# Optimization experiments

Hardware: AMD Instinct MI355X
Metric: run time of the kernel (lower is better)

## Reference

```python
import jax, jax.numpy as jnp
import numpy as np

B, S, H, NH, FF = 16, 1024, 768, 12, 3072
D = H // NH  # 64
EPS = 1e-12


def layer_norm(x, g, b):
    mu = jnp.mean(x, axis=-1, keepdims=True)
    var = jnp.mean(jnp.square(x - mu), axis=-1, keepdims=True)
    return (x - mu) * jax.lax.rsqrt(var + EPS) * g + b


def setup_inputs() -> dict:
    key = jax.random.key(0)
    ks = jax.random.split(key, 16)
    w = lambda k, shape: (jax.random.normal(k, shape, jnp.float32) * 0.02)
    return {
        "features": jax.random.normal(ks[0], (B, S, H), jnp.float32),
        "attention_mask": jnp.zeros((B, S), jnp.float32),  # additive mask
        "wq": w(ks[1], (H, H)), "bq": jnp.zeros((H,), jnp.float32),
        "wk": w(ks[2], (H, H)), "bk": jnp.zeros((H,), jnp.float32),
        "wv": w(ks[3], (H, H)), "bv": jnp.zeros((H,), jnp.float32),
        "wo": w(ks[4], (H, H)), "bo": jnp.zeros((H,), jnp.float32),
        "ln1_g": jnp.ones((H,), jnp.float32), "ln1_b": jnp.zeros((H,), jnp.float32),
        "w1": w(ks[5], (H, FF)), "b1": jnp.zeros((FF,), jnp.float32),
        "w2": w(ks[6], (FF, H)), "b2": jnp.zeros((H,), jnp.float32),
        "ln2_g": jnp.ones((H,), jnp.float32), "ln2_b": jnp.zeros((H,), jnp.float32),
        "wp": w(ks[7], (H, H)), "bp": jnp.zeros((H,), jnp.float32),
        "wm": w(ks[8], (H, 1)), "bm": jnp.zeros((1,), jnp.float32),
    }


def reference(features, attention_mask, wq, bq, wk, bk, wv, bv, wo, bo,
              ln1_g, ln1_b, w1, b1, w2, b2, ln2_g, ln2_b, wp, bp, wm, bm):
    mask = attention_mask[:, None, None, :]  # [B,1,1,S]

    def split_heads(x):  # [B,S,H] -> [B,NH,S,D]
        return x.reshape(B, S, NH, D).transpose(0, 2, 1, 3)

    q = split_heads(features @ wq + bq)
    k = split_heads(features @ wk + bk)
    v = split_heads(features @ wv + bv)

    scores = jnp.einsum("bhqd,bhkd->bhqk", q, k) / np.sqrt(D).astype(np.float32)
    probs = jax.nn.softmax(scores + mask, axis=-1)  # dropout is identity (eval)
    ctx = jnp.einsum("bhqk,bhkd->bhqd", probs, v)
    ctx = ctx.transpose(0, 2, 1, 3).reshape(B, S, H)

    attn_out = layer_norm(ctx @ wo + bo + features, ln1_g, ln1_b)
    ffn = jax.nn.gelu(attn_out @ w1 + b1, approximate=False) @ w2 + b2
    hidden = layer_norm(ffn + attn_out, ln2_g, ln2_b)

    pooled = jnp.tanh(hidden[:, 0] @ wp + bp)  # BertPooler on [CLS]
    cls = (pooled @ wm + bm).squeeze()  # [B]
    return cls
```

## Files before the change

kernel.cpp:

```cpp
#include <hip/hip_runtime.h>
#include <math.h>

namespace {

constexpr int B  = 16;
constexpr int S  = 1024;
constexpr int H  = 768;
constexpr int NH = 12;
constexpr int DH = 64;
constexpr int FF = 3072;
constexpr int KSPL = 16;
constexpr float EPS = 1e-12f;

__device__ __forceinline__ float waveReduceSum(float v) {
#pragma unroll
    for (int d = 1; d < 64; d <<= 1) v += __shfl_xor(v, d);
    return v;
}

__device__ __forceinline__ float blockReduceSum768(float v, float* red) {
    const int lane = threadIdx.x & 63;
    const int wid  = threadIdx.x >> 6;
    v = waveReduceSum(v);
    __syncthreads();
    if (lane == 0) red[wid] = v;
    __syncthreads();
    float s = 0.f;
#pragma unroll
    for (int w = 0; w < 12; ++w) s += red[w];
    return s;
}

template <int K, int ISPL, int N>
__global__ __launch_bounds__(256) void gemm_partial(
        const float* __restrict__ A, int lda, int jtOfsA,
        const float* __restrict__ W, float* __restrict__ part) {
    constexpr int IR = K / ISPL;
    __shared__ float Asl[B * IR];
    const int jt  = blockIdx.x;
    const int sp  = blockIdx.y;
    const int i0  = sp * IR;
    const int tid = threadIdx.x;

    for (int e = tid; e < B * IR; e += 256) {
        const int b = e / IR, ii = e % IR;
        Asl[e] = A[(size_t)b * lda + (size_t)jt * jtOfsA + i0 + ii];
    }
    __syncthreads();

    const int jl = tid & 63;
    const int bg = tid >> 6;
    const int j  = jt * 64 + jl;
    const float* wp_ = W + (size_t)i0 * N + j;
    const float* a0 = Asl + (bg * 4 + 0) * IR;
    const float* a1 = Asl + (bg * 4 + 1) * IR;
    const float* a2 = Asl + (bg * 4 + 2) * IR;
    const float* a3 = Asl + (bg * 4 + 3) * IR;
    float acc0 = 0.f, acc1 = 0.f, acc2 = 0.f, acc3 = 0.f;
#pragma unroll
    for (int ii = 0; ii < IR; ++ii) {
        const float w = wp_[(size_t)ii * N];
        acc0 += w * a0[ii];
        acc1 += w * a1[ii];
        acc2 += w * a2[ii];
        acc3 += w * a3[ii];
    }
    float* pp = part + ((size_t)sp * B) * N + j;
    pp[(size_t)(bg * 4 + 0) * N] = acc0;
    pp[(size_t)(bg * 4 + 1) * N] = acc1;
    pp[(size_t)(bg * 4 + 2) * N] = acc2;
    pp[(size_t)(bg * 4 + 3) * N] = acc3;
}

template <int K, int ISPL, int N, int RED>
__global__ __launch_bounds__(256) void gemm_partial_red(
        const float* __restrict__ Ain, const float* __restrict__ bias,
        const float* __restrict__ W, float* __restrict__ part) {
    constexpr int IR = K / ISPL;
    __shared__ float Asl[B * IR];
    const int jt  = blockIdx.x;
    const int sp  = blockIdx.y;
    const int i0  = sp * IR;
    const int tid = threadIdx.x;

    for (int e = tid; e < B * IR; e += 256) {
        const int b = e / IR, ii = e % IR;
        float v = bias[i0 + ii];
#pragma unroll
        for (int sp2 = 0; sp2 < RED; ++sp2)
            v += Ain[((size_t)sp2 * B + b) * K + i0 + ii];
        Asl[e] = v;
    }
    __syncthreads();

    const int jl = tid & 63;
    const int bg = tid >> 6;
    const int j  = jt * 64 + jl;
    const float* wp_ = W + (size_t)i0 * N + j;
    const float* a0 = Asl + (bg * 4 + 0) * IR;
    const float* a1 = Asl + (bg * 4 + 1) * IR;
    const float* a2 = Asl + (bg * 4 + 2) * IR;
    const float* a3 = Asl + (bg * 4 + 3) * IR;
    float acc0 = 0.f, acc1 = 0.f, acc2 = 0.f, acc3 = 0.f;
#pragma unroll
    for (int ii = 0; ii < IR; ++ii) {
        const float w = wp_[(size_t)ii * N];
        acc0 += w * a0[ii];
        acc1 += w * a1[ii];
        acc2 += w * a2[ii];
        acc3 += w * a3[ii];
    }
    float* pp = part + ((size_t)sp * B) * N + j;
    pp[(size_t)(bg * 4 + 0) * N] = acc0;
    pp[(size_t)(bg * 4 + 1) * N] = acc1;
    pp[(size_t)(bg * 4 + 2) * N] = acc2;
    pp[(size_t)(bg * 4 + 3) * N] = acc3;
}

template <int K, int ISPL, int N, int RED>
__global__ __launch_bounds__(256) void gemm_partial_red_gelu(
        const float* __restrict__ Ain, const float* __restrict__ bias,
        const float* __restrict__ W, float* __restrict__ part) {
    constexpr int IR = K / ISPL;
    __shared__ float Asl[B * IR];
    const int jt  = blockIdx.x;
    const int sp  = blockIdx.y;
    const int i0  = sp * IR;
    const int tid = threadIdx.x;

    for (int e = tid; e < B * IR; e += 256) {
        const int b = e / IR, ii = e % IR;
        float v = bias[i0 + ii];
#pragma unroll
        for (int sp2 = 0; sp2 < RED; ++sp2)
            v += Ain[((size_t)sp2 * B + b) * K + i0 + ii];
        Asl[e] = 0.5f * v * (1.0f + erff(v * 0.70710678118654752440f));
    }
    __syncthreads();

    const int jl = tid & 63;
    const int bg = tid >> 6;
    const int j  = jt * 64 + jl;
    const float* wp_ = W + (size_t)i0 * N + j;
    const float* a0 = Asl + (bg * 4 + 0) * IR;
    const float* a1 = Asl + (bg * 4 + 1) * IR;
    const float* a2 = Asl + (bg * 4 + 2) * IR;
    const float* a3 = Asl + (bg * 4 + 3) * IR;
    float acc0 = 0.f, acc1 = 0.f, acc2 = 0.f, acc3 = 0.f;
#pragma unroll 32
    for (int ii = 0; ii < IR; ++ii) {
        const float w = wp_[(size_t)ii * N];
        acc0 += w * a0[ii];
        acc1 += w * a1[ii];
        acc2 += w * a2[ii];
        acc3 += w * a3[ii];
    }
    float* pp = part + ((size_t)sp * B) * N + j;
    pp[(size_t)(bg * 4 + 0) * N] = acc0;
    pp[(size_t)(bg * 4 + 1) * N] = acc1;
    pp[(size_t)(bg * 4 + 2) * N] = acc2;
    pp[(size_t)(bg * 4 + 3) * N] = acc3;
}

template <int ISPL>
__global__ __launch_bounds__(256) void gemm_xpart(
        const float* __restrict__ xpart, const float* __restrict__ W,
        float* __restrict__ part) {
    constexpr int IR = H / ISPL;
    __shared__ float Asl[B * IR];
    const int jt  = blockIdx.x;
    const int sp  = blockIdx.y;
    const int i0  = sp * IR;
    const int tid = threadIdx.x;

    for (int e = tid; e < B * IR; e += 256) {
        const int b = e / IR, ii = e % IR;
        float v = 0.f;
#pragma unroll
        for (int s2 = 0; s2 < KSPL; ++s2)
            v += xpart[(((size_t)(b * KSPL + s2)) * NH + jt) * H + i0 + ii];
        Asl[e] = v;
    }
    __syncthreads();

    const int jl = tid & 63;
    const int bg = tid >> 6;
    const int j  = jt * 64 + jl;
    const float* wp_ = W + (size_t)i0 * H + j;
    const float* a0 = Asl + (bg * 4 + 0) * IR;
    const float* a1 = Asl + (bg * 4 + 1) * IR;
    const float* a2 = Asl + (bg * 4 + 2) * IR;
    const float* a3 = Asl + (bg * 4 + 3) * IR;
    float acc0 = 0.f, acc1 = 0.f, acc2 = 0.f, acc3 = 0.f;
#pragma unroll
    for (int ii = 0; ii < IR; ++ii) {
        const float w = wp_[(size_t)ii * H];
        acc0 += w * a0[ii];
        acc1 += w * a1[ii];
        acc2 += w * a2[ii];
        acc3 += w * a3[ii];
    }
    float* pp = part + ((size_t)sp * B) * H + j;
    pp[(size_t)(bg * 4 + 0) * H] = acc0;
    pp[(size_t)(bg * 4 + 1) * H] = acc1;
    pp[(size_t)(bg * 4 + 2) * H] = acc2;
    pp[(size_t)(bg * 4 + 3) * H] = acc3;
}

__global__ __launch_bounds__(256) void u_kernel(
        const float* __restrict__ q0_part, const float* __restrict__ bq,
        const float* __restrict__ wk, const float* __restrict__ bk,
        float* __restrict__ u, float* __restrict__ constk) {
    const int b = blockIdx.x / NH, h = blockIdx.x % NH;
    __shared__ float qh[DH];
    const int tid = threadIdx.x;
    if (tid < DH) {
        float v = bq[h * DH + tid];
#pragma unroll
        for (int sp = 0; sp < 24; ++sp)
            v += q0_part[((size_t)sp * B + b) * H + h * DH + tid];
        qh[tid] = v;
    }
    __syncthreads();
    if (tid < DH) {
        float v = bk[h * DH + tid] * qh[tid];
        v = waveReduceSum(v);
        if (tid == 0) constk[b * NH + h] = v;
    }
    const int jj = tid & 3, iq = tid >> 2;
    const float4* qv = (const float4*)qh;
    float4 q4[4];
#pragma unroll
    for (int c = 0; c < 4; ++c) q4[c] = qv[jj * 4 + c];
#pragma unroll 4
    for (int ir = 0; ir < 12; ++ir) {
        const int i = ir * 64 + iq;
        const float4* wr = (const float4*)(wk + (size_t)i * H + h * DH);
        float s = 0.f;
#pragma unroll
        for (int c = 0; c < 4; ++c) {
            const float4 w = wr[jj * 4 + c];
            s += w.x * q4[c].x + w.y * q4[c].y + w.z * q4[c].z + w.w * q4[c].w;
        }
        s += __shfl_xor(s, 1);
        s += __shfl_xor(s, 2);
        if (jj == 0) u[((size_t)(b * NH + h)) * H + i] = s;
    }
}

__global__ __launch_bounds__(256, 2) void score_kernel(
        const float* __restrict__ x, const float* __restrict__ u,
        const float* __restrict__ constk, const float* __restrict__ mask,
        float* __restrict__ e_t, float* __restrict__ psum) {
    const int b  = blockIdx.x;
    const int kt = blockIdx.y;
    __shared__ __align__(16) float ul[NH * H];
    __shared__ float ck[NH];
    __shared__ float wsum[4][NH];
    const int tid = threadIdx.x;
    {
        const float4* ug = (const float4*)(u + (size_t)b * NH * H);
        float4* ul4 = (float4*)ul;
        for (int e = tid; e < NH * H / 4; e += 256) ul4[e] = ug[e];
        if (tid < NH) ck[tid] = constk[b * NH + tid];
    }
    __syncthreads();

    const int jj = tid & 15, kk = tid >> 4;
    const int k0 = kt * 32 + kk * 2;
    float4 xv0[12], xv1[12];
    {
        const float4* xr0 = (const float4*)(x + ((size_t)b * S + k0) * H);
        const float4* xr1 = (const float4*)(x + ((size_t)b * S + k0 + 1) * H);
#pragma unroll
        for (int t = 0; t < 12; ++t) { xv0[t] = xr0[jj + 16 * t]; xv1[t] = xr1[jj + 16 * t]; }
    }
    const float4* ul4 = (const float4*)ul;
    float acc0[NH], acc1[NH];
#pragma unroll
    for (int h = 0; h < NH; ++h) {
        float a0 = 0.f, a1 = 0.f;
#pragma unroll
        for (int t = 0; t < 12; ++t) {
            const float4 uv = ul4[h * 192 + jj + 16 * t];
            a0 += xv0[t].x * uv.x + xv0[t].y * uv.y + xv0[t].z * uv.z + xv0[t].w * uv.w;
            a1 += xv1[t].x * uv.x + xv1[t].y * uv.y + xv1[t].z * uv.z + xv1[t].w * uv.w;
        }
        acc0[h] = a0; acc1[h] = a1;
    }
#pragma unroll
    for (int h = 0; h < NH; ++h) {
#pragma unroll
        for (int d = 1; d < 16; d <<= 1) {
            acc0[h] += __shfl_xor(acc0[h], d);
            acc1[h] += __shfl_xor(acc1[h], d);
        }
    }
    const float mk0 = mask[b * S + k0];
    const float mk1 = mask[b * S + k0 + 1];
    float e0[NH], e1[NH], ps[NH];
#pragma unroll
    for (int h = 0; h < NH; ++h) {
        e0[h] = expf(acc0[h] * 0.125f + ck[h] + mk0);
        e1[h] = expf(acc1[h] * 0.125f + ck[h] + mk1);
        ps[h] = e0[h] + e1[h];
    }
    if (jj == 0) {
        float4* er0 = (float4*)(e_t + ((size_t)(b * S + k0)) * NH);
        float4* er1 = (float4*)(e_t + ((size_t)(b * S + k0 + 1)) * NH);
        er0[0] = make_float4(e0[0], e0[1], e0[2], e0[3]);
        er0[1] = make_float4(e0[4], e0[5], e0[6], e0[7]);
        er0[2] = make_float4(e0[8], e0[9], e0[10], e0[11]);
        er1[0] = make_float4(e1[0], e1[1], e1[2], e1[3]);
        er1[1] = make_float4(e1[4], e1[5], e1[6], e1[7]);
        er1[2] = make_float4(e1[8], e1[9], e1[10], e1[11]);
    }
#pragma unroll
    for (int h = 0; h < NH; ++h) {
        ps[h] += __shfl_xor(ps[h], 16);
        ps[h] += __shfl_xor(ps[h], 32);
    }
    const int wid = tid >> 6;
    if ((tid & 63) == 0) {
#pragma unroll
        for (int h = 0; h < NH; ++h) wsum[wid][h] = ps[h];
    }
    __syncthreads();
    if (tid < NH)
        psum[((size_t)(b * 32 + kt)) * NH + tid] =
            wsum[0][tid] + wsum[1][tid] + wsum[2][tid] + wsum[3][tid];
}

__global__ __launch_bounds__(768) void xbar_partial(
        const float* __restrict__ x, const float* __restrict__ e_t,
        const float* __restrict__ psum, float* __restrict__ xpart) {
    constexpr int KR = S / KSPL;
    const int b = blockIdx.x, sp = blockIdx.y;
    const int tid = threadIdx.x;
    __shared__ float rinv[NH];
    if (tid < NH) {
        float s = 0.f;
#pragma unroll
        for (int kt = 0; kt < 32; ++kt) s += psum[((size_t)(b * 32 + kt)) * NH + tid];
        rinv[tid] = 1.0f / s;
    }
    float acc[NH];
#pragma unroll
    for (int h = 0; h < NH; ++h) acc[h] = 0.f;
    const float* xr = x + ((size_t)b * S + sp * KR) * H + tid;
    const float* er = e_t + ((size_t)b * S + sp * KR) * NH;
#pragma unroll 8
    for (int kk = 0; kk < KR; ++kk) {
        const float xv = xr[(size_t)kk * H];
#pragma unroll
        for (int h = 0; h < NH; ++h) acc[h] += er[kk * NH + h] * xv;
    }
    __syncthreads();
    float* op = xpart + ((size_t)(b * KSPL + sp)) * NH * H + tid;
#pragma unroll
    for (int h = 0; h < NH; ++h) op[(size_t)h * H] = acc[h] * rinv[h];
}

template <int ISPL>
__global__ __launch_bounds__(768) void ln_kernel(
        const float* __restrict__ part, const float* __restrict__ bias,
        const float* __restrict__ resid, int residStride,
        const float* __restrict__ g, const float* __restrict__ bet,
        float* __restrict__ out) {
    __shared__ float red[12];
    const int b = blockIdx.x, j = threadIdx.x;
    float v = bias[j] + resid[(size_t)b * residStride + j];
#pragma unroll
    for (int sp = 0; sp < ISPL; ++sp) v += part[((size_t)sp * B + b) * H + j];
    const float mu = blockReduceSum768(v, red) * (1.0f / H);
    const float d  = v - mu;
    const float var = blockReduceSum768(d * d, red) * (1.0f / H);
    out[(size_t)b * H + j] = d * rsqrtf(var + EPS) * g[j] + bet[j];
}

template <int ISPL>
__global__ __launch_bounds__(768) void cls_kernel(
        const float* __restrict__ part, const float* __restrict__ bp,
        const float* __restrict__ wm, const float* __restrict__ bm,
        float* __restrict__ out) {
    __shared__ float red[12];
    const int b = blockIdx.x, j = threadIdx.x;
    float v = bp[j];
#pragma unroll
    for (int sp = 0; sp < ISPL; ++sp) v += part[((size_t)sp * B + b) * H + j];
    v = tanhf(v);
    const float s = blockReduceSum768(v * wm[j], red);
    if (j == 0) out[b] = s + bm[0];
}

}

extern "C" void kernel_launch(void* const* d_in, const int* in_sizes, int n_in,
                              void* d_out, int out_size, void* d_ws, size_t ws_size,
                              hipStream_t stream) {
    const float* x    = (const float*)d_in[0];
    const float* mask = (const float*)d_in[1];
    const float* wq   = (const float*)d_in[2];
    const float* bq   = (const float*)d_in[3];
    const float* wk   = (const float*)d_in[4];
    const float* bk   = (const float*)d_in[5];
    const float* wv   = (const float*)d_in[6];
    const float* bv   = (const float*)d_in[7];
    const float* wo   = (const float*)d_in[8];
    const float* bo   = (const float*)d_in[9];
    const float* ln1g = (const float*)d_in[10];
    const float* ln1b = (const float*)d_in[11];
    const float* w1   = (const float*)d_in[12];
    const float* b1   = (const float*)d_in[13];
    const float* w2   = (const float*)d_in[14];
    const float* b2   = (const float*)d_in[15];
    const float* ln2g = (const float*)d_in[16];
    const float* ln2b = (const float*)d_in[17];
    const float* wp   = (const float*)d_in[18];
    const float* bp   = (const float*)d_in[19];
    const float* wm   = (const float*)d_in[20];
    const float* bm   = (const float*)d_in[21];
    float* out = (float*)d_out;

    float* ws = (float*)d_ws;
    size_t o = 0;
    float* u        = ws + o; o += (size_t)B * NH * H;
    float* constk   = ws + o; o += 256;
    float* e_t      = ws + o; o += (size_t)B * S * NH;
    float* psum     = ws + o; o += (size_t)B * 32 * NH;
    float* attn_out = ws + o; o += (size_t)B * H;
    float* hidden   = ws + o; o += (size_t)B * H;
    float* arena    = ws + o;
    float* q0_part   = arena;
    float* xpart     = arena;
    float* ctx_part  = arena + (size_t)KSPL * B * NH * H;
    float* wo_part   = ctx_part + (size_t)24 * B * H;
    float* ffn1_part = arena;
    float* ffn2_part = arena + (size_t)24 * B * FF;
    float* pool_part = arena;
    (void)ws_size; (void)in_sizes; (void)n_in; (void)out_size;

    gemm_partial<H, 24, H><<<dim3(12, 24), 256, 0, stream>>>(x, S * H, 0, wq, q0_part);

    u_kernel<<<B * NH, 256, 0, stream>>>(q0_part, bq, wk, bk, u, constk);

    score_kernel<<<dim3(B, S / 32), 256, 0, stream>>>(x, u, constk, mask, e_t, psum);

    xbar_partial<<<dim3(B, KSPL), 768, 0, stream>>>(x, e_t, psum, xpart);

    gemm_xpart<24><<<dim3(12, 24), 256, 0, stream>>>(xpart, wv, ctx_part);

    gemm_partial_red<H, 24, H, 24><<<dim3(12, 24), 256, 0, stream>>>(ctx_part, bv, wo, wo_part);
    ln_kernel<24><<<B, 768, 0, stream>>>(wo_part, bo, x, S * H, ln1g, ln1b, attn_out);

    gemm_partial<H, 24, FF><<<dim3(48, 24), 256, 0, stream>>>(attn_out, H, 0, w1, ffn1_part);
    gemm_partial_red_gelu<FF, 48, H, 24><<<dim3(12, 48), 256, 0, stream>>>(ffn1_part, b1, w2, ffn2_part);
    ln_kernel<48><<<B, 768, 0, stream>>>(ffn2_part, b2, attn_out, H, ln2g, ln2b, hidden);

    gemm_partial<H, 24, H><<<dim3(12, 24), 256, 0, stream>>>(hidden, H, 0, wp, pool_part);
    cls_kernel<24><<<B, 768, 0, stream>>>(pool_part, bp, wm, bm, out);
}
```

Before: 210.6 us.

## Fuse Q projection into u kernel, score with xbar, pooler with classifier

Folds the CLS query projection into the u computation, so the separate split-K GEMM launch and its partial buffer go away. The score kernel now keeps attention weights in shared memory and computes the weighted sum of x directly, which removes the e_t round trip and the xbar kernel. Softmax normalisation moves into the Wv GEMM epilogue, and the pooler GEMM is fused with the tanh/classifier reduction. In exchange, the xpart buffer grows to 32 splits, the score kernel rereads x and holds more registers, and the fused kernels run far fewer blocks with long serial loops.

```diff
diff --git a/kernel.cpp b/kernel.cpp
--- a/kernel.cpp
+++ b/kernel.cpp
@@ -9,7 +9,6 @@
 constexpr int NH = 12;
 constexpr int DH = 64;
 constexpr int FF = 3072;
-constexpr int KSPL = 16;
 constexpr float EPS = 1e-12f;
 
 __device__ __forceinline__ float waveReduceSum(float v) {
@@ -33,7 +32,7 @@
 
 template <int K, int ISPL, int N>
 __global__ __launch_bounds__(256) void gemm_partial(
-        const float* __restrict__ A, int lda, int jtOfsA,
+        const float* __restrict__ A, int lda,
         const float* __restrict__ W, float* __restrict__ part) {
     constexpr int IR = K / ISPL;
     __shared__ float Asl[B * IR];
@@ -44,7 +43,7 @@
 
     for (int e = tid; e < B * IR; e += 256) {
         const int b = e / IR, ii = e % IR;
-        Asl[e] = A[(size_t)b * lda + (size_t)jt * jtOfsA + i0 + ii];
+        Asl[e] = A[(size_t)b * lda + i0 + ii];
     }
     __syncthreads();
 
@@ -52,18 +51,14 @@
     const int bg = tid >> 6;
     const int j  = jt * 64 + jl;
     const float* wp_ = W + (size_t)i0 * N + j;
-    const float* a0 = Asl + (bg * 4 + 0) * IR;
-    const float* a1 = Asl + (bg * 4 + 1) * IR;
-    const float* a2 = Asl + (bg * 4 + 2) * IR;
-    const float* a3 = Asl + (bg * 4 + 3) * IR;
     float acc0 = 0.f, acc1 = 0.f, acc2 = 0.f, acc3 = 0.f;
 #pragma unroll
     for (int ii = 0; ii < IR; ++ii) {
         const float w = wp_[(size_t)ii * N];
-        acc0 += w * a0[ii];
-        acc1 += w * a1[ii];
-        acc2 += w * a2[ii];
-        acc3 += w * a3[ii];
+        acc0 += w * Asl[(bg * 4 + 0) * IR + ii];
+        acc1 += w * Asl[(bg * 4 + 1) * IR + ii];
+        acc2 += w * Asl[(bg * 4 + 2) * IR + ii];
+        acc3 += w * Asl[(bg * 4 + 3) * IR + ii];
     }
     float* pp = part + ((size_t)sp * B) * N + j;
     pp[(size_t)(bg * 4 + 0) * N] = acc0;
@@ -97,18 +92,14 @@
     const int bg = tid >> 6;
     const int j  = jt * 64 + jl;
     const float* wp_ = W + (size_t)i0 * N + j;
-    const float* a0 = Asl + (bg * 4 + 0) * IR;
-    const float* a1 = Asl + (bg * 4 + 1) * IR;
-    const float* a2 = Asl + (bg * 4 + 2) * IR;
-    const float* a3 = Asl + (bg * 4 + 3) * IR;
     float acc0 = 0.f, acc1 = 0.f, acc2 = 0.f, acc3 = 0.f;
 #pragma unroll
     for (int ii = 0; ii < IR; ++ii) {
         const float w = wp_[(size_t)ii * N];
-        acc0 += w * a0[ii];
-        acc1 += w * a1[ii];
-        acc2 += w * a2[ii];
-        acc3 += w * a3[ii];
+        acc0 += w * Asl[(bg * 4 + 0) * IR + ii];
+        acc1 += w * Asl[(bg * 4 + 1) * IR + ii];
+        acc2 += w * Asl[(bg * 4 + 2) * IR + ii];
+        acc3 += w * Asl[(bg * 4 + 3) * IR + ii];
     }
     float* pp = part + ((size_t)sp * B) * N + j;
     pp[(size_t)(bg * 4 + 0) * N] = acc0;
@@ -142,18 +133,14 @@
     const int bg = tid >> 6;
     const int j  = jt * 64 + jl;
     const float* wp_ = W + (size_t)i0 * N + j;
-    const float* a0 = Asl + (bg * 4 + 0) * IR;
-    const float* a1 = Asl + (bg * 4 + 1) * IR;
-    const float* a2 = Asl + (bg * 4 + 2) * IR;
-    const float* a3 = Asl + (bg * 4 + 3) * IR;
     float acc0 = 0.f, acc1 = 0.f, acc2 = 0.f, acc3 = 0.f;
 #pragma unroll 32
     for (int ii = 0; ii < IR; ++ii) {
         const float w = wp_[(size_t)ii * N];
-        acc0 += w * a0[ii];
-        acc1 += w * a1[ii];
-        acc2 += w * a2[ii];
-        acc3 += w * a3[ii];
+        acc0 += w * Asl[(bg * 4 + 0) * IR + ii];
+        acc1 += w * Asl[(bg * 4 + 1) * IR + ii];
+        acc2 += w * Asl[(bg * 4 + 2) * IR + ii];
+        acc3 += w * Asl[(bg * 4 + 3) * IR + ii];
     }
     float* pp = part + ((size_t)sp * B) * N + j;
     pp[(size_t)(bg * 4 + 0) * N] = acc0;
@@ -162,65 +149,30 @@
     pp[(size_t)(bg * 4 + 3) * N] = acc3;
 }
 
-template <int ISPL>
-__global__ __launch_bounds__(256) void gemm_xpart(
-        const float* __restrict__ xpart, const float* __restrict__ W,
-        float* __restrict__ part) {
-    constexpr int IR = H / ISPL;
-    __shared__ float Asl[B * IR];
-    const int jt  = blockIdx.x;
-    const int sp  = blockIdx.y;
-    const int i0  = sp * IR;
-    const int tid = threadIdx.x;
-
-    for (int e = tid; e < B * IR; e += 256) {
-        const int b = e / IR, ii = e % IR;
-        float v = 0.f;
-#pragma unroll
-        for (int s2 = 0; s2 < KSPL; ++s2)
-            v += xpart[(((size_t)(b * KSPL + s2)) * NH + jt) * H + i0 + ii];
-        Asl[e] = v;
-    }
-    __syncthreads();
-
-    const int jl = tid & 63;
-    const int bg = tid >> 6;
-    const int j  = jt * 64 + jl;
-    const float* wp_ = W + (size_t)i0 * H + j;
-    const float* a0 = Asl + (bg * 4 + 0) * IR;
-    const float* a1 = Asl + (bg * 4 + 1) * IR;
-    const float* a2 = Asl + (bg * 4 + 2) * IR;
-    const float* a3 = Asl + (bg * 4 + 3) * IR;
-    float acc0 = 0.f, acc1 = 0.f, acc2 = 0.f, acc3 = 0.f;
-#pragma unroll
-    for (int ii = 0; ii < IR; ++ii) {
-        const float w = wp_[(size_t)ii * H];
-        acc0 += w * a0[ii];
-        acc1 += w * a1[ii];
-        acc2 += w * a2[ii];
-        acc3 += w * a3[ii];
-    }
-    float* pp = part + ((size_t)sp * B) * H + j;
-    pp[(size_t)(bg * 4 + 0) * H] = acc0;
-    pp[(size_t)(bg * 4 + 1) * H] = acc1;
-    pp[(size_t)(bg * 4 + 2) * H] = acc2;
-    pp[(size_t)(bg * 4 + 3) * H] = acc3;
-}
-
-__global__ __launch_bounds__(256) void u_kernel(
-        const float* __restrict__ q0_part, const float* __restrict__ bq,
-        const float* __restrict__ wk, const float* __restrict__ bk,
-        float* __restrict__ u, float* __restrict__ constk) {
+__global__ __launch_bounds__(256) void qu_kernel(
+        const float* __restrict__ x, const float* __restrict__ wq,
+        const float* __restrict__ bq, const float* __restrict__ wk,
+        const float* __restrict__ bk, float* __restrict__ u,
+        float* __restrict__ constk) {
     const int b = blockIdx.x / NH, h = blockIdx.x % NH;
-    __shared__ float qh[DH];
-    const int tid = threadIdx.x;
-    if (tid < DH) {
-        float v = bq[h * DH + tid];
-#pragma unroll
-        for (int sp = 0; sp < 24; ++sp)
-            v += q0_part[((size_t)sp * B + b) * H + h * DH + tid];
-        qh[tid] = v;
-    }
+    __shared__ float xs[H];
+    __shared__ float qp[4][DH];
+    __shared__ __align__(16) float qh[DH];
+    const int tid = threadIdx.x;
+    for (int e = tid; e < H; e += 256) xs[e] = x[(size_t)b * S * H + e];
+    __syncthreads();
+    {
+        const int d = tid & 63, pr = tid >> 6;
+        float qacc = 0.f;
+        const float* wqc = wq + (size_t)(pr * 192) * H + h * DH + d;
+        const float* xsp = xs + pr * 192;
+#pragma unroll 8
+        for (int i = 0; i < 192; ++i) qacc += wqc[(size_t)i * H] * xsp[i];
+        qp[pr][d] = qacc;
+    }
+    __syncthreads();
+    if (tid < DH)
+        qh[tid] = bq[h * DH + tid] + qp[0][tid] + qp[1][tid] + qp[2][tid] + qp[3][tid];
     __syncthreads();
     if (tid < DH) {
         float v = bk[h * DH + tid] * qh[tid];
@@ -248,13 +200,14 @@
     }
 }
 
-__global__ __launch_bounds__(256, 2) void score_kernel(
+__global__ __launch_bounds__(256, 2) void score_xbar(
         const float* __restrict__ x, const float* __restrict__ u,
         const float* __restrict__ constk, const float* __restrict__ mask,
-        float* __restrict__ e_t, float* __restrict__ psum) {
+        float* __restrict__ psum, float* __restrict__ xpart) {
     const int b  = blockIdx.x;
     const int kt = blockIdx.y;
     __shared__ __align__(16) float ul[NH * H];
+    __shared__ float e_sh[32 * NH];
     __shared__ float ck[NH];
     __shared__ float wsum[4][NH];
     const int tid = threadIdx.x;
@@ -265,7 +218,6 @@
         if (tid < NH) ck[tid] = constk[b * NH + tid];
     }
     __syncthreads();
-
     const int jj = tid & 15, kk = tid >> 4;
     const int k0 = kt * 32 + kk * 2;
     float4 xv0[12], xv1[12];
@@ -306,14 +258,11 @@
         ps[h] = e0[h] + e1[h];
     }
     if (jj == 0) {
-        float4* er0 = (float4*)(e_t + ((size_t)(b * S + k0)) * NH);
-        float4* er1 = (float4*)(e_t + ((size_t)(b * S + k0 + 1)) * NH);
-        er0[0] = make_float4(e0[0], e0[1], e0[2], e0[3]);
-        er0[1] = make_float4(e0[4], e0[5], e0[6], e0[7]);
-        er0[2] = make_float4(e0[8], e0[9], e0[10], e0[11]);
-        er1[0] = make_float4(e1[0], e1[1], e1[2], e1[3]);
-        er1[1] = make_float4(e1[4], e1[5], e1[6], e1[7]);
-        er1[2] = make_float4(e1[8], e1[9], e1[10], e1[11]);
+#pragma unroll
+        for (int h = 0; h < NH; ++h) {
+            e_sh[(kk * 2) * NH + h]     = e0[h];
+            e_sh[(kk * 2 + 1) * NH + h] = e1[h];
+        }
     }
 #pragma unroll
     for (int h = 0; h < NH; ++h) {
@@ -329,36 +278,77 @@
     if (tid < NH)
         psum[((size_t)(b * 32 + kt)) * NH + tid] =
             wsum[0][tid] + wsum[1][tid] + wsum[2][tid] + wsum[3][tid];
-}
-
-__global__ __launch_bounds__(768) void xbar_partial(
-        const float* __restrict__ x, const float* __restrict__ e_t,
-        const float* __restrict__ psum, float* __restrict__ xpart) {
-    constexpr int KR = S / KSPL;
-    const int b = blockIdx.x, sp = blockIdx.y;
-    const int tid = threadIdx.x;
-    __shared__ float rinv[NH];
-    if (tid < NH) {
+
+    float aB0[NH], aB1[NH], aB2[NH];
+#pragma unroll
+    for (int h = 0; h < NH; ++h) { aB0[h] = 0.f; aB1[h] = 0.f; aB2[h] = 0.f; }
+    const float* xr = x + ((size_t)b * S + kt * 32) * H;
+#pragma unroll 2
+    for (int k = 0; k < 32; ++k) {
+        const float x0 = xr[(size_t)k * H + tid];
+        const float x1 = xr[(size_t)k * H + tid + 256];
+        const float x2 = xr[(size_t)k * H + tid + 512];
+#pragma unroll
+        for (int h = 0; h < NH; ++h) {
+            const float ev = e_sh[k * NH + h];
+            aB0[h] += ev * x0; aB1[h] += ev * x1; aB2[h] += ev * x2;
+        }
+    }
+    float* op = xpart + ((size_t)(b * 32 + kt)) * NH * H;
+#pragma unroll
+    for (int h = 0; h < NH; ++h) {
+        op[(size_t)h * H + tid]       = aB0[h];
+        op[(size_t)h * H + tid + 256] = aB1[h];
+        op[(size_t)h * H + tid + 512] = aB2[h];
+    }
+}
+
+template <int ISPL>
+__global__ __launch_bounds__(256) void gemm_xpart(
+        const float* __restrict__ xpart, const float* __restrict__ psum,
+        const float* __restrict__ W, float* __restrict__ part) {
+    constexpr int IR = H / ISPL;
+    __shared__ float Asl[B * IR];
+    __shared__ float rinv[B];
+    const int jt  = blockIdx.x;
+    const int sp  = blockIdx.y;
+    const int i0  = sp * IR;
+    const int tid = threadIdx.x;
+
+    if (tid < B) {
         float s = 0.f;
 #pragma unroll
-        for (int kt = 0; kt < 32; ++kt) s += psum[((size_t)(b * 32 + kt)) * NH + tid];
+        for (int kt = 0; kt < 32; ++kt)
+            s += psum[((size_t)(tid * 32 + kt)) * NH + jt];
         rinv[tid] = 1.0f / s;
     }
-    float acc[NH];
-#pragma unroll
-    for (int h = 0; h < NH; ++h) acc[h] = 0.f;
-    const float* xr = x + ((size_t)b * S + sp * KR) * H + tid;
-    const float* er = e_t + ((size_t)b * S + sp * KR) * NH;
-#pragma unroll 8
-    for (int kk = 0; kk < KR; ++kk) {
-        const float xv = xr[(size_t)kk * H];
-#pragma unroll
-        for (int h = 0; h < NH; ++h) acc[h] += er[kk * NH + h] * xv;
-    }
-    __syncthreads();
-    float* op = xpart + ((size_t)(b * KSPL + sp)) * NH * H + tid;
-#pragma unroll
-    for (int h = 0; h < NH; ++h) op[(size_t)h * H] = acc[h] * rinv[h];
+    for (int e = tid; e < B * IR; e += 256) {
+        const int b = e / IR, ii = e % IR;
+        float v = 0.f;
+#pragma unroll
+        for (int s2 = 0; s2 < 32; ++s2)
+            v += xpart[((size_t)(b * 32 + s2)) * NH * H + (size_t)jt * H + i0 + ii];
+        Asl[e] = v;
+    }
+    __syncthreads();
+
+    const int jl = tid & 63, bg = tid >> 6;
+    const int j = jt * 64 + jl;
+    const float* wp_ = W + (size_t)i0 * H + j;
+    float a0 = 0, a1 = 0, a2 = 0, a3 = 0;
+#pragma unroll
+    for (int ii = 0; ii < IR; ++ii) {
+        const float w = wp_[(size_t)ii * H];
+        a0 += w * Asl[(bg * 4 + 0) * IR + ii];
+        a1 += w * Asl[(bg * 4 + 1) * IR + ii];
+        a2 += w * Asl[(bg * 4 + 2) * IR + ii];
+        a3 += w * Asl[(bg * 4 + 3) * IR + ii];
+    }
+    float* pp = part + ((size_t)sp * B) * H + j;
+    pp[(size_t)(bg * 4 + 0) * H] = a0 * rinv[bg * 4 + 0];
+    pp[(size_t)(bg * 4 + 1) * H] = a1 * rinv[bg * 4 + 1];
+    pp[(size_t)(bg * 4 + 2) * H] = a2 * rinv[bg * 4 + 2];
+    pp[(size_t)(bg * 4 + 3) * H] = a3 * rinv[bg * 4 + 3];
 }
 
 template <int ISPL>
@@ -378,18 +368,20 @@
     out[(size_t)b * H + j] = d * rsqrtf(var + EPS) * g[j] + bet[j];
 }
 
-template <int ISPL>
-__global__ __launch_bounds__(768) void cls_kernel(
-        const float* __restrict__ part, const float* __restrict__ bp,
-        const float* __restrict__ wm, const float* __restrict__ bm,
-        float* __restrict__ out) {
+__global__ __launch_bounds__(768) void poolcls_kernel(
+        const float* __restrict__ hidden, const float* __restrict__ wp,
+        const float* __restrict__ bp, const float* __restrict__ wm,
+        const float* __restrict__ bm, float* __restrict__ out) {
+    __shared__ float hs[H];
     __shared__ float red[12];
     const int b = blockIdx.x, j = threadIdx.x;
-    float v = bp[j];
-#pragma unroll
-    for (int sp = 0; sp < ISPL; ++sp) v += part[((size_t)sp * B + b) * H + j];
-    v = tanhf(v);
-    const float s = blockReduceSum768(v * wm[j], red);
+    hs[j] = hidden[(size_t)b * H + j];
+    __syncthreads();
+    float acc = bp[j];
+    const float* wpc = wp + j;
+#pragma unroll 8
+    for (int i = 0; i < H; ++i) acc += wpc[(size_t)i * H] * hs[i];
+    const float s = blockReduceSum768(tanhf(acc) * wm[j], red);
     if (j == 0) out[b] = s + bm[0];
 }
 
@@ -424,39 +416,33 @@
 
     float* ws = (float*)d_ws;
     size_t o = 0;
-    float* u        = ws + o; o += (size_t)B * NH * H;
-    float* constk   = ws + o; o += 256;
-    float* e_t      = ws + o; o += (size_t)B * S * NH;
-    float* psum     = ws + o; o += (size_t)B * 32 * NH;
-    float* attn_out = ws + o; o += (size_t)B * H;
-    float* hidden   = ws + o; o += (size_t)B * H;
-    float* arena    = ws + o;
-    float* q0_part   = arena;
-    float* xpart     = arena;
-    float* ctx_part  = arena + (size_t)KSPL * B * NH * H;
-    float* wo_part   = ctx_part + (size_t)24 * B * H;
-    float* ffn1_part = arena;
-    float* ffn2_part = arena + (size_t)24 * B * FF;
-    float* pool_part = arena;
+    float* u         = ws + o; o += (size_t)B * NH * H;
+    float* constk    = ws + o; o += 256;
+    float* psum      = ws + o; o += (size_t)B * 32 * NH;
+    float* attn_out  = ws + o; o += (size_t)B * H;
+    float* hidden    = ws + o; o += (size_t)B * H;
+    float* xpart     = ws + o; o += (size_t)32 * B * NH * H;
+    float* ctx_part  = ws + o; o += (size_t)24 * B * H;
+    float* wo_part   = ws + o; o += (size_t)24 * B * H;
+    float* ffn1_part = ws + o; o += (size_t)24 * B * FF;
+    float* ffn2_part = ws + o; o += (size_t)48 * B * H;
     (void)ws_size; (void)in_sizes; (void)n_in; (void)out_size;
 
-    gemm_partial<H, 24, H><<<dim3(12, 24), 256, 0, stream>>>(x, S * H, 0, wq, q0_part);
-
-    u_kernel<<<B * NH, 256, 0, stream>>>(q0_part, bq, wk, bk, u, constk);
-
-    score_kernel<<<dim3(B, S / 32), 256, 0, stream>>>(x, u, constk, mask, e_t, psum);
-
-    xbar_partial<<<dim3(B, KSPL), 768, 0, stream>>>(x, e_t, psum, xpart);
-
-    gemm_xpart<24><<<dim3(12, 24), 256, 0, stream>>>(xpart, wv, ctx_part);
+    qu_kernel<<<B * NH, 256, 0, stream>>>(x, wq, bq, wk, bk, u, constk);
+
+    score_xbar<<<dim3(B, 32), 256, 0, stream>>>(x, u, constk, mask, psum, xpart);
+
+    gemm_xpart<24><<<dim3(12, 24), 256, 0, stream>>>(xpart, psum, wv, ctx_part);
 
     gemm_partial_red<H, 24, H, 24><<<dim3(12, 24), 256, 0, stream>>>(ctx_part, bv, wo, wo_part);
+
     ln_kernel<24><<<B, 768, 0, stream>>>(wo_part, bo, x, S * H, ln1g, ln1b, attn_out);
 
-    gemm_partial<H, 24, FF><<<dim3(48, 24), 256, 0, stream>>>(attn_out, H, 0, w1, ffn1_part);
+    gemm_partial<H, 24, FF><<<dim3(48, 24), 256, 0, stream>>>(attn_out, H, w1, ffn1_part);
+
     gemm_partial_red_gelu<FF, 48, H, 24><<<dim3(12, 48), 256, 0, stream>>>(ffn1_part, b1, w2, ffn2_part);
+
     ln_kernel<48><<<B, 768, 0, stream>>>(ffn2_part, b2, attn_out, H, ln2g, ln2b, hidden);
 
-    gemm_partial<H, 24, H><<<dim3(12, 24), 256, 0, stream>>>(hidden, H, 0, wp, pool_part);
-    cls_kernel<24><<<B, 768, 0, stream>>>(pool_part, bp, wm, bm, out);
-}
+    poolcls_kernel<<<B, 768, 0, stream>>>(hidden, wp, bp, wm, bm, out);
+}
```

Result: slower. 255.7 us (+21.4%).
